# Performance work log

Hardware: AMD Instinct MI355X
Metric: run time of the kernel (lower is better)

## Reference

```python
import math
import jax, jax.numpy as jnp
import numpy as np

B, S, D = 1, 2048, 4096
HQ, HKV = 32, 8
HD = D // HQ          # 128
N_REP = HQ // HKV     # 4
ROPE_BASE = 10000.0


def setup_inputs() -> dict:
    key = jax.random.key(0)
    ks = jax.random.split(key, 6)
    x = jax.random.normal(ks[0], (B, S, D), dtype=jnp.float32)
    scale = 0.02
    wq = jax.random.normal(ks[1], (D, HQ * HD), dtype=jnp.float32) * scale
    wk = jax.random.normal(ks[2], (D, HKV * HD), dtype=jnp.float32) * scale
    wv = jax.random.normal(ks[3], (D, HKV * HD), dtype=jnp.float32) * scale
    wo = jax.random.normal(ks[4], (HQ * HD, D), dtype=jnp.float32) * scale
    # rotary freqs: freqs_cis = exp(i * t * theta_j), theta_j = base^{-2j/hd}
    inv_freq = 1.0 / (ROPE_BASE ** (jnp.arange(0, HD, 2, dtype=jnp.float32) / HD))
    t = jnp.arange(S, dtype=jnp.float32)
    ang = t[:, None] * inv_freq[None, :]          # [S, HD/2]
    cos = jnp.cos(ang)
    sin = jnp.sin(ang)
    # additive causal mask [S, S]: 0 on/below diagonal, -1e9 above
    mask = jnp.triu(jnp.full((S, S), -1e9, dtype=jnp.float32), k=1)
    return {"x": x, "wq": wq, "wk": wk, "wv": wv, "wo": wo,
            "cos": cos, "sin": sin, "mask": mask}


def _rope(t, cos, sin):
    # t: [B, S, H, HD]; complex mult on (even, odd) pairs
    te, to = t[..., 0::2], t[..., 1::2]
    c = cos[None, :, None, :]
    s = sin[None, :, None, :]
    oe = te * c - to * s
    oo = te * s + to * c
    return jnp.stack([oe, oo], axis=-1).reshape(t.shape)


def reference(x, wq, wk, wv, wo, cos, sin, mask):
    b, s, _ = x.shape
    xq = (x @ wq).reshape(b, s, HQ, HD)
    xk = (x @ wk).reshape(b, s, HKV, HD)
    xv = (x @ wv).reshape(b, s, HKV, HD)
    xq = _rope(xq, cos, sin)
    xk = _rope(xk, cos, sin)
    # repeat_kv == repeat_interleave along head dim
    xk = jnp.repeat(xk, N_REP, axis=2)
    xv = jnp.repeat(xv, N_REP, axis=2)
    # [B, H, S, HD]
    xq = xq.transpose(0, 2, 1, 3)
    xk = xk.transpose(0, 2, 1, 3)
    xv = xv.transpose(0, 2, 1, 3)
    scores = jnp.einsum('bhqd,bhkd->bhqk', xq, xk) / math.sqrt(HD)
    scores = scores + mask[None, None, :, :]
    probs = jax.nn.softmax(scores.astype(jnp.float32), axis=-1).astype(xq.dtype)
    out = jnp.einsum('bhqk,bhkd->bhqd', probs, xv)
    out = out.transpose(0, 2, 1, 3).reshape(b, s, HQ * HD)
    return out @ wo
```

## Files before the change

kernel.cpp:

```cpp
#include <hip/hip_runtime.h>
#include <hip/hip_bf16.h>
#include <stdint.h>

#define S_LEN 2048
#define DMODEL 4096
#define N_HQ 32
#define N_HKV 8
#define HD 128
#define NQKV 6144
#define KOFF 4096
#define VOFF 5120

typedef __bf16 bf16x8 __attribute__((ext_vector_type(8)));
typedef __bf16 bf16x4 __attribute__((ext_vector_type(4)));
typedef float f32x4 __attribute__((ext_vector_type(4)));

static __device__ __forceinline__ f32x4 mfma16(bf16x8 a, bf16x8 b, f32x4 c) {
  return __builtin_amdgcn_mfma_f32_16x16x32_bf16(a, b, c, 0, 0, 0);
}

typedef const __attribute__((address_space(1))) void* gas_cvp;
typedef __attribute__((address_space(3))) void* las_vp;

__global__ __launch_bounds__(256) void cvt_f32_bf16(
    const float* __restrict__ in, __bf16* __restrict__ out)
{
  int i = blockIdx.x * 256 + threadIdx.x;
  float4 v = ((const float4*)in)[i];
  bf16x4 o = { (__bf16)v.x, (__bf16)v.y, (__bf16)v.z, (__bf16)v.w };
  *(bf16x4*)(out + 4*(size_t)i) = o;
}

__global__ __launch_bounds__(256) void transpose_cvt_k(
    const float* __restrict__ in, __bf16* __restrict__ out,
    int in_stride, int out_stride, float scale)
{
  __shared__ float tile[32][33];
  int tx = threadIdx.x & 31;
  int ty = threadIdx.x >> 5;
  size_t r0 = (size_t)blockIdx.y * 32;
  size_t c0 = (size_t)blockIdx.x * 32;
#pragma unroll
  for (int i = 0; i < 4; i++)
    tile[ty + i*8][tx] = in[(r0 + ty + i*8) * in_stride + c0 + tx];
  __syncthreads();
#pragma unroll
  for (int i = 0; i < 4; i++)
    out[(c0 + ty + i*8) * out_stride + r0 + tx] = (__bf16)(tile[tx][ty + i*8] * scale);
}

__global__ __launch_bounds__(256) void transpose_k(
    const uint16_t* __restrict__ in, uint16_t* __restrict__ out,
    int in_stride, int out_stride)
{
  __shared__ uint16_t tile[32][33];
  int tx = threadIdx.x & 31;
  int ty = threadIdx.x >> 5;
  size_t r0 = (size_t)blockIdx.y * 32;
  size_t c0 = (size_t)blockIdx.x * 32;
#pragma unroll
  for (int i = 0; i < 4; i++)
    tile[ty + i*8][tx] = in[(r0 + ty + i*8) * in_stride + c0 + tx];
  __syncthreads();
#pragma unroll
  for (int i = 0; i < 4; i++)
    out[(c0 + ty + i*8) * out_stride + r0 + tx] = tile[tx][ty + i*8];
}

#define BKG 64
template <typename OutT>
__global__ __launch_bounds__(256, 3) void gemm_bt(
    const __bf16* __restrict__ A,
    const __bf16* __restrict__ Bt,
    OutT* __restrict__ C,
    int M, int N, int K)
{
  __shared__ __attribute__((aligned(16))) __bf16 Asl[128*BKG];
  __shared__ __attribute__((aligned(16))) __bf16 Bsl[128*BKG];
  int tid = threadIdx.x;
  int lane = tid & 63, wave = tid >> 6;
  int wm = wave >> 1, wn = wave & 1;
  int row16 = lane & 15, quad = lane >> 4;
  size_t m0 = (size_t)blockIdx.y * 128;
  size_t n0 = (size_t)blockIdx.x * 128;
  f32x4 acc[4][4] = {};

  for (int k0 = 0; k0 < K; k0 += BKG) {
    __syncthreads();
#pragma unroll
    for (int c = 0; c < 4; c++) {
      int u = c*256 + tid;
      int r = u >> 3;
      int swz = (u & 7) ^ (r & 7);
      const __bf16* ga = A + (m0 + r) * (size_t)K + k0 + swz*8;
      char* la = (char*)Asl + (size_t)(c*256 + wave*64) * 16;
      __builtin_amdgcn_global_load_lds((gas_cvp)ga, (las_vp)la, 16, 0, 0);
      const __bf16* gb = Bt + (n0 + r) * (size_t)K + k0 + swz*8;
      char* lb = (char*)Bsl + (size_t)(c*256 + wave*64) * 16;
      __builtin_amdgcn_global_load_lds((gas_cvp)gb, (las_vp)lb, 16, 0, 0);
    }
    __syncthreads();

#pragma unroll
    for (int kk = 0; kk < 2; kk++) {
      int sw = ((kk*4 + quad) ^ (row16 & 7)) * 8;
      bf16x8 af[4], bfr[4];
#pragma unroll
      for (int i = 0; i < 4; i++)
        af[i] = *(const bf16x8*)&Asl[(wm*64 + i*16 + row16)*BKG + sw];
#pragma unroll
      for (int j = 0; j < 4; j++)
        bfr[j] = *(const bf16x8*)&Bsl[(wn*64 + j*16 + row16)*BKG + sw];
#pragma unroll
      for (int i = 0; i < 4; i++)
#pragma unroll
        for (int j = 0; j < 4; j++)
          acc[i][j] = mfma16(af[i], bfr[j], acc[i][j]);
    }
  }

#pragma unroll
  for (int i = 0; i < 4; i++)
#pragma unroll
    for (int j = 0; j < 4; j++)
#pragma unroll
      for (int r = 0; r < 4; r++) {
        size_t row = m0 + wm*64 + i*16 + quad*4 + r;
        size_t col = n0 + wn*64 + j*16 + row16;
        C[row * (size_t)N + col] = (OutT)acc[i][j][r];
      }
}

__global__ __launch_bounds__(256) void rope_k(
    __bf16* __restrict__ qkv,
    const float* __restrict__ cosb,
    const float* __restrict__ sinb)
{
  int idx = blockIdx.x * 256 + threadIdx.x;
  const int NQP = S_LEN * N_HQ * 64;
  __bf16* p;
  int s, i;
  if (idx < NQP) {
    s = idx >> 11;
    int rem = idx & 2047;
    int h = rem >> 6;
    i = rem & 63;
    p = qkv + (size_t)s * NQKV + h*HD + 2*i;
  } else {
    int j = idx - NQP;
    s = j >> 9;
    int rem = j & 511;
    int h = rem >> 6;
    i = rem & 63;
    p = qkv + (size_t)s * NQKV + KOFF + h*HD + 2*i;
  }
  float te = (float)p[0], to = (float)p[1];
  float c = cosb[s*64 + i], sn = sinb[s*64 + i];
  p[0] = (__bf16)(te*c - to*sn);
  p[1] = (__bf16)(te*sn + to*c);
}

#define KB 64
#define KSTR 136
#define VSTR 72
__global__ __launch_bounds__(256, 2) void attn_k(
    const __bf16* __restrict__ qkv,
    const __bf16* __restrict__ vt,
    __bf16* __restrict__ attnout)
{
  __shared__ __attribute__((aligned(16))) __bf16 Kl[KB*KSTR];
  __shared__ __attribute__((aligned(16))) __bf16 Vl[HD*VSTR];
  __shared__ __attribute__((aligned(16))) __bf16 Pl[4*32*VSTR];
  int tid = threadIdx.x;
  int lane = tid & 63, wave = tid >> 6;
  int row16 = lane & 15, quad = lane >> 4;

  int b = blockIdx.x;
  int i = b & 255;
  int h = i & 31;
  int qt = (b >> 8) ? (i >> 5) : (15 - (i >> 5));
  int hkv = h >> 2;
  int wq0 = qt*128 + wave*32;
  int nkt = 2*qt + 2;
  int ktd = 2*qt + (wave >> 1);

  bf16x8 qf[2][4];
#pragma unroll
  for (int mt = 0; mt < 2; mt++)
#pragma unroll
    for (int c = 0; c < 4; c++)
      qf[mt][c] = *(const bf16x8*)&qkv[(size_t)(wq0 + mt*16 + row16)*NQKV + h*HD + c*32 + quad*8];

  f32x4 acc[2][8] = {};
  float lsum[2][4] = {};

  __bf16* Pw = &Pl[wave*32*VSTR];
  for (int kt = 0; kt < nkt; kt++) {
    int kb = kt*KB;
    __syncthreads();
#pragma unroll
    for (int c = 0; c < 4; c++) {
      int u = tid + c*256;
      int kl = u >> 4, doff = (u & 15)*8;
      *(uint4*)&Kl[kl*KSTR + doff] =
        *(const uint4*)&qkv[(size_t)(kb+kl)*NQKV + KOFF + hkv*HD + doff];
      int dd = u >> 3, part = u & 7;
      *(uint4*)&Vl[dd*VSTR + part*8] =
        *(const uint4*)&vt[(size_t)(hkv*HD + dd)*S_LEN + kb + part*8];
    }
    __syncthreads();
    if (kt > ktd) continue;

    f32x4 s[2][4] = {};
#pragma unroll
    for (int c = 0; c < 4; c++) {
      bf16x8 kf[4];
#pragma unroll
      for (int jt = 0; jt < 4; jt++)
        kf[jt] = *(const bf16x8*)&Kl[(jt*16 + row16)*KSTR + c*32 + quad*8];
#pragma unroll
      for (int mt = 0; mt < 2; mt++)
#pragma unroll
        for (int jt = 0; jt < 4; jt++)
          s[mt][jt] = mfma16(qf[mt][c], kf[jt], s[mt][jt]);
    }

    if (kt == ktd) {
#pragma unroll
      for (int mt = 0; mt < 2; mt++)
#pragma unroll
        for (int r = 0; r < 4; r++) {
          int rowl = mt*16 + quad*4 + r;
          int row_g = wq0 + rowl;
#pragma unroll
          for (int jt = 0; jt < 4; jt++) {
            int col_g = kb + jt*16 + row16;
            float e = (col_g <= row_g) ? exp2f(s[mt][jt][r]) : 0.0f;
            lsum[mt][r] += e;
            Pw[rowl*VSTR + jt*16 + row16] = (__bf16)e;
          }
        }
    } else {
#pragma unroll
      for (int mt = 0; mt < 2; mt++)
#pragma unroll
        for (int r = 0; r < 4; r++) {
          int rowl = mt*16 + quad*4 + r;
#pragma unroll
          for (int jt = 0; jt < 4; jt++) {
            float e = exp2f(s[mt][jt][r]);
            lsum[mt][r] += e;
            Pw[rowl*VSTR + jt*16 + row16] = (__bf16)e;
          }
        }
    }

#pragma unroll
    for (int kk = 0; kk < 2; kk++) {
      bf16x8 pa0 = *(const bf16x8*)&Pw[(row16)*VSTR + kk*32 + quad*8];
      bf16x8 pa1 = *(const bf16x8*)&Pw[(16+row16)*VSTR + kk*32 + quad*8];
#pragma unroll
      for (int ct = 0; ct < 8; ct++) {
        bf16x8 vb = *(const bf16x8*)&Vl[(ct*16 + row16)*VSTR + kk*32 + quad*8];
        acc[0][ct] = mfma16(pa0, vb, acc[0][ct]);
        acc[1][ct] = mfma16(pa1, vb, acc[1][ct]);
      }
    }
  }

#pragma unroll
  for (int mt = 0; mt < 2; mt++)
#pragma unroll
    for (int r = 0; r < 4; r++) {
      float l = lsum[mt][r];
      l += __shfl_xor(l, 1);
      l += __shfl_xor(l, 2);
      l += __shfl_xor(l, 4);
      l += __shfl_xor(l, 8);
      lsum[mt][r] = 1.0f / l;
    }
#pragma unroll
  for (int mt = 0; mt < 2; mt++)
#pragma unroll
    for (int r = 0; r < 4; r++) {
      size_t qrow = (size_t)wq0 + mt*16 + quad*4 + r;
      float inv = lsum[mt][r];
#pragma unroll
      for (int ct = 0; ct < 8; ct++)
        attnout[qrow*DMODEL + h*HD + ct*16 + row16] = (__bf16)(acc[mt][ct][r] * inv);
    }
}

extern "C" void kernel_launch(void* const* d_in, const int* in_sizes, int n_in,
                              void* d_out, int out_size, void* d_ws, size_t ws_size,
                              hipStream_t stream) {
  const float* x    = (const float*)d_in[0];
  const float* wq   = (const float*)d_in[1];
  const float* wk   = (const float*)d_in[2];
  const float* wv   = (const float*)d_in[3];
  const float* wo   = (const float*)d_in[4];
  const float* cosb = (const float*)d_in[5];
  const float* sinb = (const float*)d_in[6];
  float* out = (float*)d_out;

  __bf16* ws   = (__bf16*)d_ws;
  __bf16* Wt   = ws;
  __bf16* Wot  = ws;
  __bf16* xb   = Wt  + (size_t)NQKV*DMODEL;
  __bf16* attn = xb;
  __bf16* qkv  = xb  + (size_t)S_LEN*DMODEL;
  __bf16* vt   = qkv + (size_t)S_LEN*NQKV;

  const float QSCALE = 0.12751295866442674f;

  cvt_f32_bf16<<<8192,256,0,stream>>>(x, xb);
  transpose_cvt_k<<<dim3(128,128),256,0,stream>>>(wq, Wt, 4096, 4096, QSCALE);
  transpose_cvt_k<<<dim3(32,128),256,0,stream>>>(wk, Wt + (size_t)4096*4096, 1024, 4096, 1.0f);
  transpose_cvt_k<<<dim3(32,128),256,0,stream>>>(wv, Wt + (size_t)5120*4096, 1024, 4096, 1.0f);

  gemm_bt<__bf16><<<dim3(NQKV/128, S_LEN/128),256,0,stream>>>(xb, Wt, qkv, S_LEN, NQKV, DMODEL);

  rope_k<<<20480,256,0,stream>>>(qkv, cosb, sinb);

  transpose_k<<<dim3(32,64),256,0,stream>>>((const uint16_t*)(qkv + VOFF), (uint16_t*)vt, NQKV, S_LEN);

  transpose_cvt_k<<<dim3(128,128),256,0,stream>>>(wo, Wot, 4096, 4096, 1.0f);

  attn_k<<<512,256,0,stream>>>(qkv, vt, attn);

  gemm_bt<float><<<dim3(DMODEL/128, S_LEN/128),256,0,stream>>>(attn, Wot, out, S_LEN, DMODEL, DMODEL);
}
```

Measured before the change: 544.2 us.

## Pair heavy and light query tiles per block and stage K/V via swizzled direct-to-LDS loads

Each attention block now holds one 16-row slice from a late (heavy) query tile and one from the matching early (light) tile, so every block does roughly the same causal work. The light-tile MFMAs are skipped once past its diagonal. K/V staging switches to global_load_lds with an XOR swizzle in place of padded LDS rows, which avoids register round-trips and bank conflicts. The light half idles for most iterations, and the branching on lightOn adds divergence-free but serial overhead.

```diff
diff --git a/kernel.cpp b/kernel.cpp
--- a/kernel.cpp
+++ b/kernel.cpp
@@ -161,109 +161,145 @@
 }
 
 #define KB 64
-#define KSTR 136
-#define VSTR 72
+#define PSTR 72
 __global__ __launch_bounds__(256, 2) void attn_k(
     const __bf16* __restrict__ qkv,
     const __bf16* __restrict__ vt,
     __bf16* __restrict__ attnout)
 {
-  __shared__ __attribute__((aligned(16))) __bf16 Kl[KB*KSTR];
-  __shared__ __attribute__((aligned(16))) __bf16 Vl[HD*VSTR];
-  __shared__ __attribute__((aligned(16))) __bf16 Pl[4*32*VSTR];
+  __shared__ __attribute__((aligned(16))) __bf16 Kl[KB*HD];
+  __shared__ __attribute__((aligned(16))) __bf16 Vl[HD*KB];
+  __shared__ __attribute__((aligned(16))) __bf16 Pl[4*32*PSTR];
   int tid = threadIdx.x;
   int lane = tid & 63, wave = tid >> 6;
   int row16 = lane & 15, quad = lane >> 4;
 
   int b = blockIdx.x;
-  int i = b & 255;
-  int h = i & 31;
-  int qt = (b >> 8) ? (i >> 5) : (15 - (i >> 5));
+  int h = b & 31;
+  int j = b >> 5;
+  int pr = j >> 1, hb = j & 1;
+  int qt_h = 15 - pr;
+  int qt_l = pr;
   int hkv = h >> 2;
-  int wq0 = qt*128 + wave*32;
-  int nkt = 2*qt + 2;
-  int ktd = 2*qt + (wave >> 1);
+  int h0 = qt_h*128 + hb*64 + wave*16;
+  int l0 = qt_l*128 + hb*64 + wave*16;
+  int ktd_h = 2*qt_h + hb;
+  int ktd_l = 2*qt_l + hb;
+  int nkt = ktd_h + 1;
 
   bf16x8 qf[2][4];
 #pragma unroll
-  for (int mt = 0; mt < 2; mt++)
-#pragma unroll
-    for (int c = 0; c < 4; c++)
-      qf[mt][c] = *(const bf16x8*)&qkv[(size_t)(wq0 + mt*16 + row16)*NQKV + h*HD + c*32 + quad*8];
+  for (int c = 0; c < 4; c++) {
+    qf[0][c] = *(const bf16x8*)&qkv[(size_t)(h0 + row16)*NQKV + h*HD + c*32 + quad*8];
+    qf[1][c] = *(const bf16x8*)&qkv[(size_t)(l0 + row16)*NQKV + h*HD + c*32 + quad*8];
+  }
 
   f32x4 acc[2][8] = {};
   float lsum[2][4] = {};
 
-  __bf16* Pw = &Pl[wave*32*VSTR];
+  __bf16* Pw = &Pl[wave*32*PSTR];
   for (int kt = 0; kt < nkt; kt++) {
     int kb = kt*KB;
     __syncthreads();
 #pragma unroll
     for (int c = 0; c < 4; c++) {
-      int u = tid + c*256;
-      int kl = u >> 4, doff = (u & 15)*8;
-      *(uint4*)&Kl[kl*KSTR + doff] =
-        *(const uint4*)&qkv[(size_t)(kb+kl)*NQKV + KOFF + hkv*HD + doff];
-      int dd = u >> 3, part = u & 7;
-      *(uint4*)&Vl[dd*VSTR + part*8] =
-        *(const uint4*)&vt[(size_t)(hkv*HD + dd)*S_LEN + kb + part*8];
+      int u = c*256 + tid;
+      int kr = u >> 4;
+      int kp = (u & 15) ^ (kr & 15);
+      const __bf16* gk = &qkv[(size_t)(kb+kr)*NQKV + KOFF + hkv*HD + kp*8];
+      char* lk = (char*)Kl + (size_t)(c*256 + wave*64) * 16;
+      __builtin_amdgcn_global_load_lds((gas_cvp)gk, (las_vp)lk, 16, 0, 0);
+      int dd = u >> 3;
+      int vp = (u & 7) ^ (dd & 7);
+      const __bf16* gv = &vt[(size_t)(hkv*HD + dd)*S_LEN + kb + vp*8];
+      char* lv = (char*)Vl + (size_t)(c*256 + wave*64) * 16;
+      __builtin_amdgcn_global_load_lds((gas_cvp)gv, (las_vp)lv, 16, 0, 0);
     }
     __syncthreads();
-    if (kt > ktd) continue;
+
+    int lightOn = (kt <= ktd_l);
 
     f32x4 s[2][4] = {};
 #pragma unroll
     for (int c = 0; c < 4; c++) {
       bf16x8 kf[4];
 #pragma unroll
+      for (int jt = 0; jt < 4; jt++) {
+        int pc = (c*4 + quad) ^ row16;
+        kf[jt] = *(const bf16x8*)&Kl[(jt*16 + row16)*HD + pc*8];
+      }
+#pragma unroll
       for (int jt = 0; jt < 4; jt++)
-        kf[jt] = *(const bf16x8*)&Kl[(jt*16 + row16)*KSTR + c*32 + quad*8];
-#pragma unroll
-      for (int mt = 0; mt < 2; mt++)
+        s[0][jt] = mfma16(qf[0][c], kf[jt], s[0][jt]);
+      if (lightOn)
 #pragma unroll
         for (int jt = 0; jt < 4; jt++)
-          s[mt][jt] = mfma16(qf[mt][c], kf[jt], s[mt][jt]);
-    }
-
-    if (kt == ktd) {
-#pragma unroll
-      for (int mt = 0; mt < 2; mt++)
+          s[1][jt] = mfma16(qf[1][c], kf[jt], s[1][jt]);
+    }
+
+    if (kt == ktd_h) {
+#pragma unroll
+      for (int r = 0; r < 4; r++) {
+        int rowl = quad*4 + r;
+        int row_g = h0 + rowl;
+#pragma unroll
+        for (int jt = 0; jt < 4; jt++) {
+          int col_g = kb + jt*16 + row16;
+          float e = (col_g <= row_g) ? exp2f(s[0][jt][r]) : 0.0f;
+          lsum[0][r] += e;
+          Pw[rowl*PSTR + jt*16 + row16] = (__bf16)e;
+        }
+      }
+    } else {
+#pragma unroll
+      for (int r = 0; r < 4; r++) {
+        int rowl = quad*4 + r;
+#pragma unroll
+        for (int jt = 0; jt < 4; jt++) {
+          float e = exp2f(s[0][jt][r]);
+          lsum[0][r] += e;
+          Pw[rowl*PSTR + jt*16 + row16] = (__bf16)e;
+        }
+      }
+    }
+    if (lightOn) {
+      if (kt == ktd_l) {
 #pragma unroll
         for (int r = 0; r < 4; r++) {
-          int rowl = mt*16 + quad*4 + r;
-          int row_g = wq0 + rowl;
+          int rowl = quad*4 + r;
+          int row_g = l0 + rowl;
 #pragma unroll
           for (int jt = 0; jt < 4; jt++) {
             int col_g = kb + jt*16 + row16;
-            float e = (col_g <= row_g) ? exp2f(s[mt][jt][r]) : 0.0f;
-            lsum[mt][r] += e;
-            Pw[rowl*VSTR + jt*16 + row16] = (__bf16)e;
+            float e = (col_g <= row_g) ? exp2f(s[1][jt][r]) : 0.0f;
+            lsum[1][r] += e;
+            Pw[(16+rowl)*PSTR + jt*16 + row16] = (__bf16)e;
           }
         }
-    } else {
-#pragma unroll
-      for (int mt = 0; mt < 2; mt++)
+      } else {
 #pragma unroll
         for (int r = 0; r < 4; r++) {
-          int rowl = mt*16 + quad*4 + r;
+          int rowl = quad*4 + r;
 #pragma unroll
           for (int jt = 0; jt < 4; jt++) {
-            float e = exp2f(s[mt][jt][r]);
-            lsum[mt][r] += e;
-            Pw[rowl*VSTR + jt*16 + row16] = (__bf16)e;
+            float e = exp2f(s[1][jt][r]);
+            lsum[1][r] += e;
+            Pw[(16+rowl)*PSTR + jt*16 + row16] = (__bf16)e;
           }
         }
+      }
     }
 
 #pragma unroll
     for (int kk = 0; kk < 2; kk++) {
-      bf16x8 pa0 = *(const bf16x8*)&Pw[(row16)*VSTR + kk*32 + quad*8];
-      bf16x8 pa1 = *(const bf16x8*)&Pw[(16+row16)*VSTR + kk*32 + quad*8];
+      bf16x8 pa0 = *(const bf16x8*)&Pw[(row16)*PSTR + kk*32 + quad*8];
+      bf16x8 pa1 = *(const bf16x8*)&Pw[(16+row16)*PSTR + kk*32 + quad*8];
 #pragma unroll
       for (int ct = 0; ct < 8; ct++) {
-        bf16x8 vb = *(const bf16x8*)&Vl[(ct*16 + row16)*VSTR + kk*32 + quad*8];
+        int pv = (kk*4 + quad) ^ (row16 & 7);
+        bf16x8 vb = *(const bf16x8*)&Vl[(ct*16 + row16)*KB + pv*8];
         acc[0][ct] = mfma16(pa0, vb, acc[0][ct]);
-        acc[1][ct] = mfma16(pa1, vb, acc[1][ct]);
+        if (lightOn) acc[1][ct] = mfma16(pa1, vb, acc[1][ct]);
       }
     }
   }
@@ -280,15 +316,17 @@
       lsum[mt][r] = 1.0f / l;
     }
 #pragma unroll
-  for (int mt = 0; mt < 2; mt++)
+  for (int mt = 0; mt < 2; mt++) {
+    int base = (mt == 0) ? h0 : l0;
 #pragma unroll
     for (int r = 0; r < 4; r++) {
-      size_t qrow = (size_t)wq0 + mt*16 + quad*4 + r;
+      size_t qrow = (size_t)base + quad*4 + r;
       float inv = lsum[mt][r];
 #pragma unroll
       for (int ct = 0; ct < 8; ct++)
         attnout[qrow*DMODEL + h*HD + ct*16 + row16] = (__bf16)(acc[mt][ct][r] * inv);
     }
+  }
 }
 
 extern "C" void kernel_launch(void* const* d_in, const int* in_sizes, int n_in,
```

Measured after the change: 488.2 us. 1.11x faster.
